# Performance work log

Measured on AMD Instinct MI355X. Metric: run time of the kernel, lower is better.

The kernel has to match this reference:

```python
import jax, jax.numpy as jnp
import numpy as np

N_NODES = 50000


def gcn_conv(x, src, dst, W, b):
    # PyG GCNConv: h = x @ W; symmetric norm with added self-loops; out = A_hat h + b
    h = x @ W
    deg = jax.ops.segment_sum(jnp.ones_like(src, dtype=h.dtype), dst,
                              num_segments=N_NODES) + 1.0  # +1 self-loop
    dis = jax.lax.rsqrt(deg)  # deg >= 1, safe
    msg = h[src] * (dis[src] * dis[dst])[:, None]          # [E,H] gather + scale
    agg = jax.ops.segment_sum(msg, dst, num_segments=N_NODES)
    agg = agg + h * (dis * dis)[:, None]                   # self-loop contribution
    return agg + b


def link_pred(zs, e, Wp, bp):
    # zs: [L,N,H]; gather endpoints along node dim, per-edge cross-layer Gram matrix
    s = zs[:, e[0]]                                # [L,E,H]
    d = zs[:, e[1]]                                # [L,E,H]
    dot = jnp.einsum('leh,meh->elm', s, d)         # [E,L,L] per-edge bmm
    emb = dot.reshape(dot.shape[0], -1)            # [E,L*L]
    return emb @ Wp + bp                           # [E,1] logits (activation=False)


def reference(x, ei, pos, neg, W0, b0, Wh, bh, Wp, bp):
    src, dst = ei[0], ei[1]
    h = jax.nn.relu(gcn_conv(x, src, dst, W0, b0))
    embs = [h]
    for i in range(Wh.shape[0]):  # fixed small layer count
        h = jax.nn.relu(gcn_conv(h, src, dst, Wh[i], bh[i]))
        embs.append(h)
    zs = jnp.stack(embs, axis=0)                   # [L,N,H]
    pos_pred = link_pred(zs, pos, Wp, bp)
    neg_pred = link_pred(zs, neg, Wp, bp)
    logits = jnp.concatenate([pos_pred, neg_pred], axis=0)  # [2E,1]
    # faithful to source: targets all zero except row index == n_pos set to 1
    targets = jnp.zeros_like(logits).at[pos_pred.shape[0]].set(1.0)
    # BCEWithLogitsLoss (mean, numerically stable)
    loss = jnp.mean(jnp.clip(logits, 0.0) - logits * targets
                    + jnp.log1p(jnp.exp(-jnp.abs(logits))))
    return loss


def setup_inputs():
    key = jax.random.key(0)
    ks = jax.random.split(key, 10)
    N, E, EP, IN, H, L = 50000, 800000, 100000, 128, 64, 4
    x = jax.random.normal(ks[0], (N, IN), jnp.float32)
    ei = jax.random.randint(ks[1], (2, E), 0, N, dtype=jnp.int32)
    pos = jax.random.randint(ks[2], (2, EP), 0, N, dtype=jnp.int32)
    neg = jax.random.randint(ks[3], (2, EP), 0, N, dtype=jnp.int32)
    def u(k, shape, fan_in):
        s = 1.0 / np.sqrt(fan_in)
        return jax.random.uniform(k, shape, jnp.float32, -s, s)
    W0 = u(ks[4], (IN, H), IN)
    b0 = u(ks[5], (H,), IN)
    Wh = u(ks[6], (L - 1, H, H), H)
    bh = u(ks[7], (L - 1, H), H)
    Wp = u(ks[8], (L * L, 1), L * L)
    bp = u(ks[9], (1,), L * L)
    return {"x": x, "ei": ei, "pos": pos, "neg": neg, "W0": W0, "b0": b0,
            "Wh": Wh, "bh": bh, "Wp": Wp, "bp": bp}
```

## Files before the change

kernel.cpp:

```cpp
#include <hip/hip_runtime.h>
#include <hip/hip_bf16.h>
#include <math.h>

constexpr int N_NODES = 50000;
constexpr int HD = 64;
constexpr int NBKT = (N_NODES + 255) / 256;

typedef float floatx2 __attribute__((ext_vector_type(2)));

__device__ __forceinline__ float bf2f(unsigned short u) {
    return __uint_as_float((unsigned)u << 16);
}
__device__ __forceinline__ unsigned short f2bf(float f) {
    __hip_bfloat16 b = __float2bfloat16(f);
    return *(unsigned short*)&b;
}
__device__ __forceinline__ unsigned pack_fp8x4(float a, float b, float c, float d) {
    unsigned p = __builtin_amdgcn_cvt_pk_fp8_f32(a, b, 0u, false);
    return __builtin_amdgcn_cvt_pk_fp8_f32(c, d, p, true);
}

__global__ __launch_bounds__(256) void bhist_kernel(const int* __restrict__ dst,
                                                    int* __restrict__ bcnt, int E) {
    __shared__ int lh[256];
    const int t = threadIdx.x;
    lh[t] = 0;
    __syncthreads();
    const int beg = blockIdx.x * 2048;
    const int end = min(beg + 2048, E);
    for (int i = beg + t; i < end; i += 256)
        atomicAdd(&lh[dst[i] >> 8], 1);
    __syncthreads();
    if (t < NBKT && lh[t]) atomicAdd(&bcnt[t], lh[t]);
}

__global__ __launch_bounds__(256) void bscan_kernel(const int* __restrict__ bcnt,
                                                    int* __restrict__ bbase,
                                                    int* __restrict__ gcur) {
    const int t = threadIdx.x;
    const int v = (t < NBKT) ? bcnt[t] : 0;
    const int lane = t & 63, wid = t >> 6;
    int incl = v;
#pragma unroll
    for (int o = 1; o <= 32; o <<= 1) {
        int u = __shfl_up(incl, o);
        if (lane >= o) incl += u;
    }
    __shared__ int wt[4];
    if (lane == 63) wt[wid] = incl;
    __syncthreads();
    int base = 0;
    for (int w = 0; w < wid; ++w) base += wt[w];
    const int excl = base + incl - v;
    if (t < NBKT) { bbase[t] = excl; gcur[t] = excl; }
    if (t == NBKT - 1) bbase[NBKT] = excl + v;
}

__global__ __launch_bounds__(256) void partition_kernel(const int* __restrict__ src,
                                                        const int* __restrict__ dst,
                                                        int* __restrict__ gcur,
                                                        unsigned* __restrict__ pk, int E) {
    __shared__ unsigned epk[8192];
    __shared__ int lh[NBKT], lbase[NBKT], lcur[NBKT];
    const int t = threadIdx.x;
    for (int i = t; i < NBKT; i += 256) { lh[i] = 0; lcur[i] = 0; }
    __syncthreads();
    const int beg = blockIdx.x * 8192;
    const int end = min(beg + 8192, E);
    for (int i = beg + t; i < end; i += 256) {
        const int s = src[i], d = dst[i];
        const int bkt = d >> 8;
        epk[i - beg] = ((unsigned)bkt << 24) | ((unsigned)(d & 255) << 16) | (unsigned)s;
        atomicAdd(&lh[bkt], 1);
    }
    __syncthreads();
    for (int i = t; i < NBKT; i += 256)
        if (lh[i]) lbase[i] = atomicAdd(&gcur[i], lh[i]);
    __syncthreads();
    for (int i = beg + t; i < end; i += 256) {
        const unsigned p = epk[i - beg];
        const int bkt = p >> 24;
        const int r = atomicAdd(&lcur[bkt], 1);
        pk[lbase[bkt] + r] = p;
    }
}

__global__ __launch_bounds__(256) void bsort_kernel(const unsigned* __restrict__ pk,
                                                    const int* __restrict__ bbase,
                                                    int* __restrict__ off,
                                                    float* __restrict__ dis,
                                                    int* __restrict__ csr, int E, int N) {
    __shared__ int ncnt[256], nbs[256], ncur[256];
    __shared__ int wt[4];
    const int t = threadIdx.x;
    const int bkt = blockIdx.x;
    const int gb = bbase[bkt], ge = bbase[bkt + 1];
    ncnt[t] = 0; ncur[t] = 0;
    __syncthreads();
    for (int i = gb + t; i < ge; i += 256)
        atomicAdd(&ncnt[(pk[i] >> 16) & 255], 1);
    __syncthreads();
    const int v = ncnt[t];
    const int lane = t & 63, wid = t >> 6;
    int incl = v;
#pragma unroll
    for (int o = 1; o <= 32; o <<= 1) {
        int u = __shfl_up(incl, o);
        if (lane >= o) incl += u;
    }
    if (lane == 63) wt[wid] = incl;
    __syncthreads();
    int base = 0;
    for (int w = 0; w < wid; ++w) base += wt[w];
    nbs[t] = base + incl - v;
    const int n = bkt * 256 + t;
    if (n < N) {
        off[n] = gb + nbs[t];
        dis[n] = rsqrtf((float)v + 1.0f);
        if (n == N - 1) off[N] = E;
    }
    __syncthreads();
    for (int i = gb + t; i < ge; i += 256) {
        const unsigned p = pk[i];
        const int dl = (p >> 16) & 255;
        const int r = atomicAdd(&ncur[dl], 1);
        csr[gb + nbs[dl] + r] = (int)(p & 0xFFFFu);
    }
}

template <int K, bool INBF16>
__global__ __launch_bounds__(256) void gemm_kernel(const void* __restrict__ in_,
                                                   const float* __restrict__ W,
                                                   unsigned short* __restrict__ out16,
                                                   unsigned* __restrict__ out8, int N) {
    __shared__ float xs[64][68];
    __shared__ float Wl[64][64];
    const int t = threadIdx.x;
    const int row0 = blockIdx.x * 64;
    const int cq = t & 15, rq = t >> 4;
    float acc[4][4] = {{0.f}};
    for (int kc = 0; kc < K; kc += 64) {
#pragma unroll
        for (int it = 0; it < 4; ++it) {
            const int idx = it * 256 + t;
            const int r = idx >> 4, c4 = idx & 15;
            const int rr = min(row0 + r, N - 1);
            if constexpr (INBF16) {
                const unsigned short* in16 = (const unsigned short*)in_;
                const ushort4 v = *(const ushort4*)(in16 + (size_t)rr * K + kc + c4 * 4);
                *(float4*)(&xs[r][c4 * 4]) = make_float4(bf2f(v.x), bf2f(v.y), bf2f(v.z), bf2f(v.w));
            } else {
                const float* inf = (const float*)in_;
                *(float4*)(&xs[r][c4 * 4]) = *(const float4*)(inf + (size_t)rr * K + kc + c4 * 4);
            }
            *(float4*)(&Wl[r][c4 * 4]) = *(const float4*)(W + (size_t)(kc + r) * HD + c4 * 4);
        }
        __syncthreads();
#pragma unroll
        for (int k4 = 0; k4 < 16; ++k4) {
            float a[4][4], b[4][4];
#pragma unroll
            for (int i = 0; i < 4; ++i)
                *(float4*)a[i] = *(const float4*)(&xs[rq * 4 + i][k4 * 4]);
#pragma unroll
            for (int kk = 0; kk < 4; ++kk)
                *(float4*)b[kk] = *(const float4*)(&Wl[k4 * 4 + kk][cq * 4]);
#pragma unroll
            for (int kk = 0; kk < 4; ++kk)
#pragma unroll
                for (int i = 0; i < 4; ++i)
#pragma unroll
                    for (int j = 0; j < 4; ++j)
                        acc[i][j] = fmaf(a[i][kk], b[kk][j], acc[i][j]);
        }
        __syncthreads();
    }
#pragma unroll
    for (int i = 0; i < 4; ++i) {
        const int r = row0 + rq * 4 + i;
        if (r < N) {
            ushort4 o;
            o.x = f2bf(acc[i][0]); o.y = f2bf(acc[i][1]);
            o.z = f2bf(acc[i][2]); o.w = f2bf(acc[i][3]);
            *(ushort4*)(out16 + (size_t)r * HD + cq * 4) = o;
            out8[(size_t)r * 16 + cq] = pack_fp8x4(acc[i][0], acc[i][1], acc[i][2], acc[i][3]);
        }
    }
}

__global__ __launch_bounds__(256) void agg_kernel(const int* __restrict__ csr,
                                                  const int* __restrict__ off,
                                                  const float* __restrict__ dis,
                                                  const unsigned short* __restrict__ h16,
                                                  const unsigned* __restrict__ h8,
                                                  const float* __restrict__ b,
                                                  unsigned short* __restrict__ z16, int N) {
    const int lane = threadIdx.x & 63;
    const int wid  = threadIdx.x >> 6;
    const int n = blockIdx.x * 4 + wid;
    if (n >= N) return;
    const int beg = off[n];
    const int c = min(off[n + 1] - beg, 64);
    int   s_l = 0;
    float w_l = 0.f;
    if (lane < c) {
        s_l = csr[beg + lane];
        w_l = dis[s_l];
    }
    const float dn = dis[n];
    const int g = lane >> 3;
    const int p = lane & 7;
    float a[8];
#pragma unroll
    for (int j = 0; j < 8; ++j) a[j] = 0.f;
    int   sE = __shfl(s_l, g);
    float wE = __shfl(w_l, g);
    uint2 hv = *(const uint2*)(h8 + (size_t)sE * 16 + p * 2);
    for (int e = 8; e < c; e += 8) {
        const int   sN = __shfl(s_l, e + g);
        const float wN = __shfl(w_l, e + g);
        const uint2 nv = *(const uint2*)(h8 + (size_t)sN * 16 + p * 2);
        floatx2 f01 = __builtin_amdgcn_cvt_pk_f32_fp8(hv.x, false);
        floatx2 f23 = __builtin_amdgcn_cvt_pk_f32_fp8(hv.x, true);
        floatx2 f45 = __builtin_amdgcn_cvt_pk_f32_fp8(hv.y, false);
        floatx2 f67 = __builtin_amdgcn_cvt_pk_f32_fp8(hv.y, true);
        a[0] = fmaf(f01[0], wE, a[0]); a[1] = fmaf(f01[1], wE, a[1]);
        a[2] = fmaf(f23[0], wE, a[2]); a[3] = fmaf(f23[1], wE, a[3]);
        a[4] = fmaf(f45[0], wE, a[4]); a[5] = fmaf(f45[1], wE, a[5]);
        a[6] = fmaf(f67[0], wE, a[6]); a[7] = fmaf(f67[1], wE, a[7]);
        hv = nv; wE = wN;
    }
    {
        floatx2 f01 = __builtin_amdgcn_cvt_pk_f32_fp8(hv.x, false);
        floatx2 f23 = __builtin_amdgcn_cvt_pk_f32_fp8(hv.x, true);
        floatx2 f45 = __builtin_amdgcn_cvt_pk_f32_fp8(hv.y, false);
        floatx2 f67 = __builtin_amdgcn_cvt_pk_f32_fp8(hv.y, true);
        a[0] = fmaf(f01[0], wE, a[0]); a[1] = fmaf(f01[1], wE, a[1]);
        a[2] = fmaf(f23[0], wE, a[2]); a[3] = fmaf(f23[1], wE, a[3]);
        a[4] = fmaf(f45[0], wE, a[4]); a[5] = fmaf(f45[1], wE, a[5]);
        a[6] = fmaf(f67[0], wE, a[6]); a[7] = fmaf(f67[1], wE, a[7]);
    }
#pragma unroll
    for (int st = 8; st <= 32; st <<= 1)
#pragma unroll
        for (int j = 0; j < 8; ++j) a[j] += __shfl_xor(a[j], st);
    if (g == 0) {
        const uint4 sv = *(const uint4*)(h16 + (size_t)n * HD + p * 8);
        const unsigned ss[4] = {sv.x, sv.y, sv.z, sv.w};
        const float4 b0 = *(const float4*)(b + p * 8);
        const float4 b1 = *(const float4*)(b + p * 8 + 4);
        const float bb[8] = {b0.x, b0.y, b0.z, b0.w, b1.x, b1.y, b1.z, b1.w};
        float o[8];
#pragma unroll
        for (int q = 0; q < 4; ++q) {
            o[2 * q]     = a[2 * q]     + __uint_as_float(ss[q] << 16) * dn;
            o[2 * q + 1] = a[2 * q + 1] + __uint_as_float(ss[q] & 0xFFFF0000u) * dn;
        }
#pragma unroll
        for (int j = 0; j < 8; ++j) o[j] = fmaxf(fmaf(o[j], dn, bb[j]), 0.f);
        ushort4 o0, o1;
        o0.x = f2bf(o[0]); o0.y = f2bf(o[1]); o0.z = f2bf(o[2]); o0.w = f2bf(o[3]);
        o1.x = f2bf(o[4]); o1.y = f2bf(o[5]); o1.z = f2bf(o[6]); o1.w = f2bf(o[7]);
        unsigned short* zp = z16 + (size_t)n * HD + p * 8;
        *(ushort4*)zp = o0;
        *(ushort4*)(zp + 4) = o1;
    }
}

__global__ __launch_bounds__(256) void uprep_kernel(const unsigned short* __restrict__ z16,
                                                    const float* __restrict__ Wp,
                                                    unsigned* __restrict__ u8,
                                                    unsigned* __restrict__ d8, int N) {
    const int i = blockIdx.x * blockDim.x + threadIdx.x;
    const int total = N * HD;
    if (i >= total) return;
    const size_t NH = (size_t)N_NODES * HD;
    const float z0 = bf2f(z16[0 * NH + i]), z1 = bf2f(z16[1 * NH + i]);
    const float z2 = bf2f(z16[2 * NH + i]), z3 = bf2f(z16[3 * NH + i]);
    d8[i] = pack_fp8x4(z0, z1, z2, z3);
    const float u0 = z0 * Wp[0] + z1 * Wp[4] + z2 * Wp[8]  + z3 * Wp[12];
    const float u1 = z0 * Wp[1] + z1 * Wp[5] + z2 * Wp[9]  + z3 * Wp[13];
    const float u2 = z0 * Wp[2] + z1 * Wp[6] + z2 * Wp[10] + z3 * Wp[14];
    const float u3 = z0 * Wp[3] + z1 * Wp[7] + z2 * Wp[11] + z3 * Wp[15];
    u8[i] = pack_fp8x4(u0, u1, u2, u3);
}

__global__ __launch_bounds__(256) void linkpred_kernel(const unsigned* __restrict__ u8,
                                                       const unsigned* __restrict__ d8,
                                                       const int* __restrict__ pos,
                                                       const int* __restrict__ neg,
                                                       const float* __restrict__ bp,
                                                       double* __restrict__ acc, int EP) {
    const int lane = threadIdx.x & 63;
    const int wid  = threadIdx.x >> 6;
    const float bpv = bp[0];
    int gw = blockIdx.x * 4 + wid;
    const int nw = gridDim.x * 4;
    const int nchunks = (2 * EP) >> 3;
    float lsum = 0.f;
    for (int c0 = gw; c0 < nchunks; c0 += nw) {
        const int c = __builtin_amdgcn_readfirstlane(c0);
        const int i0 = c << 3;
        const bool is_pos = i0 < EP;
        const int* __restrict__ eptr = is_pos ? pos : neg;
        const int jj0 = is_pos ? i0 : i0 - EP;
        float t[8];
#pragma unroll
        for (int k = 0; k < 8; ++k) {
            const int e0 = eptr[jj0 + k];
            const int e1 = eptr[EP + jj0 + k];
            const unsigned uv = u8[(size_t)e0 * HD + lane];
            const unsigned dv = d8[(size_t)e1 * HD + lane];
            floatx2 ua = __builtin_amdgcn_cvt_pk_f32_fp8(uv, false);
            floatx2 ub = __builtin_amdgcn_cvt_pk_f32_fp8(uv, true);
            floatx2 da = __builtin_amdgcn_cvt_pk_f32_fp8(dv, false);
            floatx2 db = __builtin_amdgcn_cvt_pk_f32_fp8(dv, true);
            float s = ua[0] * da[0];
            s = fmaf(ua[1], da[1], s);
            s = fmaf(ub[0], db[0], s);
            s = fmaf(ub[1], db[1], s);
            t[k] = s;
        }
#pragma unroll
        for (int st = 1; st <= 32; st <<= 1) {
#pragma unroll
            for (int k = 0; k < 8; ++k) t[k] += __shfl_xor(t[k], st);
        }
        if (lane < 8) {
            float tt = t[0];
            tt = (lane == 1) ? t[1] : tt;
            tt = (lane == 2) ? t[2] : tt;
            tt = (lane == 3) ? t[3] : tt;
            tt = (lane == 4) ? t[4] : tt;
            tt = (lane == 5) ? t[5] : tt;
            tt = (lane == 6) ? t[6] : tt;
            tt = (lane == 7) ? t[7] : tt;
            float logit  = tt + bpv;
            float target = (i0 + lane == EP) ? 1.f : 0.f;
            lsum += fmaxf(logit, 0.f) - logit * target + log1pf(expf(-fabsf(logit)));
        }
    }
#pragma unroll
    for (int o = 32; o >= 1; o >>= 1) lsum += __shfl_xor(lsum, o);
    __shared__ float wsum[4];
    if (lane == 0) wsum[wid] = lsum;
    __syncthreads();
    if (threadIdx.x == 0) {
        double bs = (double)wsum[0] + (double)wsum[1] + (double)wsum[2] + (double)wsum[3];
        atomicAdd(acc, bs);
    }
}

__global__ void loss_final(const double* __restrict__ acc, float* __restrict__ out, int denom) {
    out[0] = (float)(acc[0] / (double)denom);
}

extern "C" void kernel_launch(void* const* d_in, const int* in_sizes, int n_in,
                              void* d_out, int out_size, void* d_ws, size_t ws_size,
                              hipStream_t stream) {
    const float* x   = (const float*)d_in[0];
    const int*   ei  = (const int*)d_in[1];
    const int*   pos = (const int*)d_in[2];
    const int*   neg = (const int*)d_in[3];
    const float* W0  = (const float*)d_in[4];
    const float* b0  = (const float*)d_in[5];
    const float* Wh  = (const float*)d_in[6];
    const float* bh  = (const float*)d_in[7];
    const float* Wp  = (const float*)d_in[8];
    const float* bp  = (const float*)d_in[9];
    const int E  = in_sizes[1] / 2;
    const int EP = in_sizes[2] / 2;
    const int N  = N_NODES;
    const size_t NH = (size_t)N * HD;

    char* ws = (char*)d_ws;
    size_t off_b = 0;
    auto alloc = [&](size_t bytes) { char* p = ws + off_b; off_b = (off_b + bytes + 255) & ~(size_t)255; return p; };
    unsigned short* h16 = (unsigned short*)alloc(NH * sizeof(unsigned short));
    unsigned*       h8  = (unsigned*)alloc(NH);
    unsigned short* z16 = (unsigned short*)alloc(4 * NH * sizeof(unsigned short));
    unsigned*       u8  = (unsigned*)alloc(NH * sizeof(unsigned));
    unsigned*       d8  = (unsigned*)alloc(NH * sizeof(unsigned));
    float* dis = (float*)alloc((size_t)N * sizeof(float));
    int*   off = (int*)alloc((size_t)(N + 1) * sizeof(int));
    int*   csr = (int*)alloc((size_t)E * sizeof(int));
    unsigned* pk = (unsigned*)alloc((size_t)E * sizeof(unsigned));
    int*   bbase = (int*)alloc((size_t)(NBKT + 1) * sizeof(int));
    int*   gcur  = (int*)alloc((size_t)NBKT * sizeof(int));
    char*  zbase = ws + off_b;
    int*   bcnt = (int*)alloc((size_t)NBKT * sizeof(int));
    double* acc = (double*)alloc(sizeof(double));
    size_t zero_bytes = (size_t)((char*)acc - zbase) + sizeof(double);

    hipMemsetAsync(zbase, 0, zero_bytes, stream);

    const int* src = ei;
    const int* dst = ei + E;

    bhist_kernel<<<(E + 2047) / 2048, 256, 0, stream>>>(dst, bcnt, E);
    bscan_kernel<<<1, 256, 0, stream>>>(bcnt, bbase, gcur);
    partition_kernel<<<(E + 8191) / 8192, 256, 0, stream>>>(src, dst, gcur, pk, E);
    bsort_kernel<<<NBKT, 256, 0, stream>>>(pk, bbase, off, dis, csr, E, N);

    const int agg_blocks  = (N + 3) / 4;
    const int gemm_blocks = (N + 63) / 64;

    gemm_kernel<128, false><<<gemm_blocks, 256, 0, stream>>>(x, W0, h16, h8, N);
    agg_kernel<<<agg_blocks, 256, 0, stream>>>(csr, off, dis, h16, h8, b0, z16, N);

    for (int l = 1; l < 4; ++l) {
        unsigned short* zprev = z16 + (size_t)(l - 1) * NH;
        unsigned short* zcur  = z16 + (size_t)l * NH;
        gemm_kernel<64, true><<<gemm_blocks, 256, 0, stream>>>(zprev, Wh + (size_t)(l - 1) * HD * HD, h16, h8, N);
        agg_kernel<<<agg_blocks, 256, 0, stream>>>(csr, off, dis, h16, h8,
                                                   bh + (size_t)(l - 1) * HD, zcur, N);
    }

    uprep_kernel<<<(N * HD + 255) / 256, 256, 0, stream>>>(z16, Wp, u8, d8, N);
    linkpred_kernel<<<2048, 256, 0, stream>>>(u8, d8, pos, neg, bp, acc, EP);
    loss_final<<<1, 1, 0, stream>>>(acc, (float*)d_out, 2 * EP);
}
```

Baseline: 275.7 us.

## Prescale GEMM output by source norm, drop bf16 copy, use 16-bit CSR

The GEMM now multiplies each row by dis[r] before packing to fp8 and writes only the fp8 buffer. This removes the bf16 h copy, and aggregation no longer gathers dis[src] per edge or does FMAs. The self-loop term now comes from the fp8 prescaled row instead of bf16, which lowers its precision. A zeroed sentinel row N replaces masking for out-of-range lanes. The CSR indices are stored as 16-bit values, which truncates node ids above 65535; that is fine for N=50000. Partition chunk size and linkpred grid size are also retuned.

```diff
diff --git a/kernel.cpp b/kernel.cpp
--- a/kernel.cpp
+++ b/kernel.cpp
@@ -60,13 +60,13 @@
                                                         const int* __restrict__ dst,
                                                         int* __restrict__ gcur,
                                                         unsigned* __restrict__ pk, int E) {
-    __shared__ unsigned epk[8192];
+    __shared__ unsigned epk[4096];
     __shared__ int lh[NBKT], lbase[NBKT], lcur[NBKT];
     const int t = threadIdx.x;
     for (int i = t; i < NBKT; i += 256) { lh[i] = 0; lcur[i] = 0; }
     __syncthreads();
-    const int beg = blockIdx.x * 8192;
-    const int end = min(beg + 8192, E);
+    const int beg = blockIdx.x * 4096;
+    const int end = min(beg + 4096, E);
     for (int i = beg + t; i < end; i += 256) {
         const int s = src[i], d = dst[i];
         const int bkt = d >> 8;
@@ -89,7 +89,7 @@
                                                     const int* __restrict__ bbase,
                                                     int* __restrict__ off,
                                                     float* __restrict__ dis,
-                                                    int* __restrict__ csr, int E, int N) {
+                                                    unsigned short* __restrict__ csr, int E, int N) {
     __shared__ int ncnt[256], nbs[256], ncur[256];
     __shared__ int wt[4];
     const int t = threadIdx.x;
@@ -124,14 +124,14 @@
         const unsigned p = pk[i];
         const int dl = (p >> 16) & 255;
         const int r = atomicAdd(&ncur[dl], 1);
-        csr[gb + nbs[dl] + r] = (int)(p & 0xFFFFu);
+        csr[gb + nbs[dl] + r] = (unsigned short)(p & 0xFFFFu);
     }
 }
 
 template <int K, bool INBF16>
 __global__ __launch_bounds__(256) void gemm_kernel(const void* __restrict__ in_,
                                                    const float* __restrict__ W,
-                                                   unsigned short* __restrict__ out16,
+                                                   const float* __restrict__ dis,
                                                    unsigned* __restrict__ out8, int N) {
     __shared__ float xs[64][68];
     __shared__ float Wl[64][64];
@@ -179,20 +179,17 @@
     for (int i = 0; i < 4; ++i) {
         const int r = row0 + rq * 4 + i;
         if (r < N) {
-            ushort4 o;
-            o.x = f2bf(acc[i][0]); o.y = f2bf(acc[i][1]);
-            o.z = f2bf(acc[i][2]); o.w = f2bf(acc[i][3]);
-            *(ushort4*)(out16 + (size_t)r * HD + cq * 4) = o;
-            out8[(size_t)r * 16 + cq] = pack_fp8x4(acc[i][0], acc[i][1], acc[i][2], acc[i][3]);
-        }
-    }
-}
-
-__global__ __launch_bounds__(256) void agg_kernel(const int* __restrict__ csr,
+            const float dr = dis[r];
+            out8[(size_t)r * 16 + cq] =
+                pack_fp8x4(acc[i][0] * dr, acc[i][1] * dr, acc[i][2] * dr, acc[i][3] * dr);
+        }
+    }
+}
+
+__global__ __launch_bounds__(256) void agg_kernel(const unsigned short* __restrict__ csr,
                                                   const int* __restrict__ off,
                                                   const float* __restrict__ dis,
-                                                  const unsigned short* __restrict__ h16,
-                                                  const unsigned* __restrict__ h8,
+                                                  const unsigned* __restrict__ hs,
                                                   const float* __restrict__ b,
                                                   unsigned short* __restrict__ z16, int N) {
     const int lane = threadIdx.x & 63;
@@ -201,63 +198,53 @@
     if (n >= N) return;
     const int beg = off[n];
     const int c = min(off[n + 1] - beg, 64);
-    int   s_l = 0;
-    float w_l = 0.f;
-    if (lane < c) {
-        s_l = csr[beg + lane];
-        w_l = dis[s_l];
-    }
+    int s_l = N;
+    if (lane < c) s_l = csr[beg + lane];
     const float dn = dis[n];
     const int g = lane >> 3;
     const int p = lane & 7;
     float a[8];
 #pragma unroll
     for (int j = 0; j < 8; ++j) a[j] = 0.f;
-    int   sE = __shfl(s_l, g);
-    float wE = __shfl(w_l, g);
-    uint2 hv = *(const uint2*)(h8 + (size_t)sE * 16 + p * 2);
+    int sE = __shfl(s_l, g);
+    uint2 hv = *(const uint2*)(hs + (size_t)sE * 16 + p * 2);
     for (int e = 8; e < c; e += 8) {
-        const int   sN = __shfl(s_l, e + g);
-        const float wN = __shfl(w_l, e + g);
-        const uint2 nv = *(const uint2*)(h8 + (size_t)sN * 16 + p * 2);
+        const int sN = __shfl(s_l, e + g);
+        const uint2 nv = *(const uint2*)(hs + (size_t)sN * 16 + p * 2);
         floatx2 f01 = __builtin_amdgcn_cvt_pk_f32_fp8(hv.x, false);
         floatx2 f23 = __builtin_amdgcn_cvt_pk_f32_fp8(hv.x, true);
         floatx2 f45 = __builtin_amdgcn_cvt_pk_f32_fp8(hv.y, false);
         floatx2 f67 = __builtin_amdgcn_cvt_pk_f32_fp8(hv.y, true);
-        a[0] = fmaf(f01[0], wE, a[0]); a[1] = fmaf(f01[1], wE, a[1]);
-        a[2] = fmaf(f23[0], wE, a[2]); a[3] = fmaf(f23[1], wE, a[3]);
-        a[4] = fmaf(f45[0], wE, a[4]); a[5] = fmaf(f45[1], wE, a[5]);
-        a[6] = fmaf(f67[0], wE, a[6]); a[7] = fmaf(f67[1], wE, a[7]);
-        hv = nv; wE = wN;
+        a[0] += f01[0]; a[1] += f01[1]; a[2] += f23[0]; a[3] += f23[1];
+        a[4] += f45[0]; a[5] += f45[1]; a[6] += f67[0]; a[7] += f67[1];
+        hv = nv;
     }
     {
         floatx2 f01 = __builtin_amdgcn_cvt_pk_f32_fp8(hv.x, false);
         floatx2 f23 = __builtin_amdgcn_cvt_pk_f32_fp8(hv.x, true);
         floatx2 f45 = __builtin_amdgcn_cvt_pk_f32_fp8(hv.y, false);
         floatx2 f67 = __builtin_amdgcn_cvt_pk_f32_fp8(hv.y, true);
-        a[0] = fmaf(f01[0], wE, a[0]); a[1] = fmaf(f01[1], wE, a[1]);
-        a[2] = fmaf(f23[0], wE, a[2]); a[3] = fmaf(f23[1], wE, a[3]);
-        a[4] = fmaf(f45[0], wE, a[4]); a[5] = fmaf(f45[1], wE, a[5]);
-        a[6] = fmaf(f67[0], wE, a[6]); a[7] = fmaf(f67[1], wE, a[7]);
+        a[0] += f01[0]; a[1] += f01[1]; a[2] += f23[0]; a[3] += f23[1];
+        a[4] += f45[0]; a[5] += f45[1]; a[6] += f67[0]; a[7] += f67[1];
     }
 #pragma unroll
     for (int st = 8; st <= 32; st <<= 1)
 #pragma unroll
         for (int j = 0; j < 8; ++j) a[j] += __shfl_xor(a[j], st);
     if (g == 0) {
-        const uint4 sv = *(const uint4*)(h16 + (size_t)n * HD + p * 8);
-        const unsigned ss[4] = {sv.x, sv.y, sv.z, sv.w};
+        const uint2 sv = *(const uint2*)(hs + (size_t)n * 16 + p * 2);
+        floatx2 s01 = __builtin_amdgcn_cvt_pk_f32_fp8(sv.x, false);
+        floatx2 s23 = __builtin_amdgcn_cvt_pk_f32_fp8(sv.x, true);
+        floatx2 s45 = __builtin_amdgcn_cvt_pk_f32_fp8(sv.y, false);
+        floatx2 s67 = __builtin_amdgcn_cvt_pk_f32_fp8(sv.y, true);
+        a[0] += s01[0]; a[1] += s01[1]; a[2] += s23[0]; a[3] += s23[1];
+        a[4] += s45[0]; a[5] += s45[1]; a[6] += s67[0]; a[7] += s67[1];
         const float4 b0 = *(const float4*)(b + p * 8);
         const float4 b1 = *(const float4*)(b + p * 8 + 4);
         const float bb[8] = {b0.x, b0.y, b0.z, b0.w, b1.x, b1.y, b1.z, b1.w};
         float o[8];
 #pragma unroll
-        for (int q = 0; q < 4; ++q) {
-            o[2 * q]     = a[2 * q]     + __uint_as_float(ss[q] << 16) * dn;
-            o[2 * q + 1] = a[2 * q + 1] + __uint_as_float(ss[q] & 0xFFFF0000u) * dn;
-        }
-#pragma unroll
-        for (int j = 0; j < 8; ++j) o[j] = fmaxf(fmaf(o[j], dn, bb[j]), 0.f);
+        for (int j = 0; j < 8; ++j) o[j] = fmaxf(fmaf(a[j], dn, bb[j]), 0.f);
         ushort4 o0, o1;
         o0.x = f2bf(o[0]); o0.y = f2bf(o[1]); o0.z = f2bf(o[2]); o0.w = f2bf(o[3]);
         o1.x = f2bf(o[4]); o1.y = f2bf(o[5]); o1.z = f2bf(o[6]); o1.w = f2bf(o[7]);
@@ -376,14 +363,13 @@
     char* ws = (char*)d_ws;
     size_t off_b = 0;
     auto alloc = [&](size_t bytes) { char* p = ws + off_b; off_b = (off_b + bytes + 255) & ~(size_t)255; return p; };
-    unsigned short* h16 = (unsigned short*)alloc(NH * sizeof(unsigned short));
-    unsigned*       h8  = (unsigned*)alloc(NH);
+    unsigned*       hs  = (unsigned*)alloc((size_t)(N + 1) * 16 * sizeof(unsigned));
     unsigned short* z16 = (unsigned short*)alloc(4 * NH * sizeof(unsigned short));
     unsigned*       u8  = (unsigned*)alloc(NH * sizeof(unsigned));
     unsigned*       d8  = (unsigned*)alloc(NH * sizeof(unsigned));
     float* dis = (float*)alloc((size_t)N * sizeof(float));
     int*   off = (int*)alloc((size_t)(N + 1) * sizeof(int));
-    int*   csr = (int*)alloc((size_t)E * sizeof(int));
+    unsigned short* csr = (unsigned short*)alloc((size_t)E * sizeof(unsigned short));
     unsigned* pk = (unsigned*)alloc((size_t)E * sizeof(unsigned));
     int*   bbase = (int*)alloc((size_t)(NBKT + 1) * sizeof(int));
     int*   gcur  = (int*)alloc((size_t)NBKT * sizeof(int));
@@ -393,30 +379,31 @@
     size_t zero_bytes = (size_t)((char*)acc - zbase) + sizeof(double);
 
     hipMemsetAsync(zbase, 0, zero_bytes, stream);
+    hipMemsetAsync(hs + (size_t)N * 16, 0, 16 * sizeof(unsigned), stream);
 
     const int* src = ei;
     const int* dst = ei + E;
 
     bhist_kernel<<<(E + 2047) / 2048, 256, 0, stream>>>(dst, bcnt, E);
     bscan_kernel<<<1, 256, 0, stream>>>(bcnt, bbase, gcur);
-    partition_kernel<<<(E + 8191) / 8192, 256, 0, stream>>>(src, dst, gcur, pk, E);
+    partition_kernel<<<(E + 4095) / 4096, 256, 0, stream>>>(src, dst, gcur, pk, E);
     bsort_kernel<<<NBKT, 256, 0, stream>>>(pk, bbase, off, dis, csr, E, N);
 
     const int agg_blocks  = (N + 3) / 4;
     const int gemm_blocks = (N + 63) / 64;
 
-    gemm_kernel<128, false><<<gemm_blocks, 256, 0, stream>>>(x, W0, h16, h8, N);
-    agg_kernel<<<agg_blocks, 256, 0, stream>>>(csr, off, dis, h16, h8, b0, z16, N);
+    gemm_kernel<128, false><<<gemm_blocks, 256, 0, stream>>>(x, W0, dis, hs, N);
+    agg_kernel<<<agg_blocks, 256, 0, stream>>>(csr, off, dis, hs, b0, z16, N);
 
     for (int l = 1; l < 4; ++l) {
         unsigned short* zprev = z16 + (size_t)(l - 1) * NH;
         unsigned short* zcur  = z16 + (size_t)l * NH;
-        gemm_kernel<64, true><<<gemm_blocks, 256, 0, stream>>>(zprev, Wh + (size_t)(l - 1) * HD * HD, h16, h8, N);
-        agg_kernel<<<agg_blocks, 256, 0, stream>>>(csr, off, dis, h16, h8,
+        gemm_kernel<64, true><<<gemm_blocks, 256, 0, stream>>>(zprev, Wh + (size_t)(l - 1) * HD * HD, dis, hs, N);
+        agg_kernel<<<agg_blocks, 256, 0, stream>>>(csr, off, dis, hs,
                                                    bh + (size_t)(l - 1) * HD, zcur, N);
     }
 
     uprep_kernel<<<(N * HD + 255) / 256, 256, 0, stream>>>(z16, Wp, u8, d8, N);
-    linkpred_kernel<<<2048, 256, 0, stream>>>(u8, d8, pos, neg, bp, acc, EP);
+    linkpred_kernel<<<3125, 256, 0, stream>>>(u8, d8, pos, neg, bp, acc, EP);
     loss_final<<<1, 1, 0, stream>>>(acc, (float*)d_out, 2 * EP);
 }
```

After: 299.6 us. 1.09x slower.
